# Kernel optimization log

Measured on AMD Instinct MI355X. Metric: run time of the kernel, lower is better.

The kernel has to match this reference:

```python
import jax, jax.numpy as jnp
import numpy as np

NUM_HEADS = 8

def setup_inputs() -> dict:
    key0 = jax.random.key(0)
    ks = jax.random.split(key0, 12)
    L, S, N, E, Dh = 1024, 1024, 8, 512, 64
    w_scale = 1.0 / np.sqrt(E)
    return {
        "query": jax.random.normal(ks[0], (L, N, E), jnp.float32),
        "key": jax.random.normal(ks[1], (S, N, E), jnp.float32),
        "value": jax.random.normal(ks[2], (S, N, E), jnp.float32),
        "pos_k": jax.random.normal(ks[3], (L, S, Dh), jnp.float32) * 0.1,
        "pos_v": jax.random.normal(ks[4], (L, S, Dh), jnp.float32) * 0.1,
        "Wq": jax.random.normal(ks[5], (E, E), jnp.float32) * w_scale,
        "bq": jnp.zeros((E,), jnp.float32),
        "Wk": jax.random.normal(ks[6], (E, E), jnp.float32) * w_scale,
        "bk": jnp.zeros((E,), jnp.float32),
        "Wv": jax.random.normal(ks[7], (E, E), jnp.float32) * w_scale,
        "bv": jnp.zeros((E,), jnp.float32),
        "Wo": jax.random.normal(ks[8], (E, E), jnp.float32) * w_scale,
        "bo": jnp.zeros((E,), jnp.float32),
    }


def reference(query, key, value, pos_k, pos_v, Wq, bq, Wk, bk, Wv, bv, Wo, bo):
    L, N, E = query.shape
    S = key.shape[0]
    H = NUM_HEADS
    Dh = E // H
    scaling = Dh ** -0.5

    # separate Q/K/V projections (torch Linear: x @ W.T + b)
    q = (query @ Wq.T + bq) * scaling          # (L, N, E)
    k = key @ Wk.T + bk                        # (S, N, E)
    v = value @ Wv.T + bv                      # (S, N, E)

    # (L, N*H, Dh) -> (N*H, L, Dh), matching torch's view+transpose
    q = q.reshape(L, N * H, Dh).transpose(1, 0, 2)
    k = k.reshape(S, N * H, Dh).transpose(1, 0, 2)
    v = v.reshape(S, N * H, Dh).transpose(1, 0, 2)

    # content scores + relative-position key term B
    scores = jnp.einsum('bld,bsd->bls', q, k)          # (N*H, L, S)
    scores = scores + jnp.einsum('bld,lsd->bls', q, pos_k)

    # mine_softmax: clamp to finfo.min (turns -inf into finite min), then softmax
    scores = jnp.maximum(scores, jnp.finfo(scores.dtype).min)
    w = jax.nn.softmax(scores, axis=-1)                # (N*H, L, S)

    # attention output + relative-position value term
    out = jnp.einsum('bls,bsd->bld', w, v) + jnp.einsum('bls,lsd->bld', w, pos_v)
    out = out.transpose(1, 0, 2).reshape(L, N, E)
    attn_output = out @ Wo.T + bo                      # (L, N, E)

    # averaged attention weights over heads: (N, L, S)
    avg_w = w.reshape(N, H, L, S).sum(axis=1) / H
    return attn_output, avg_w
```

## Files before the change

### kernel.cpp

```cpp
#include <hip/hip_runtime.h>
#include <hip/hip_bf16.h>
#include <hip/hip_fp16.h>


typedef float     f32x4  __attribute__((ext_vector_type(4)));
typedef _Float16  f16x8  __attribute__((ext_vector_type(8)));

#define MFMA_F16  __builtin_amdgcn_mfma_f32_16x16x32_f16

__device__ __forceinline__ f16x8 ld8f(const float* __restrict__ p){
  const f32x4 a = *(const f32x4*)p;
  const f32x4 b = *(const f32x4*)(p + 4);
  f16x8 h;
#pragma unroll
  for (int t = 0; t < 4; ++t) { h[t] = (_Float16)a[t]; h[t + 4] = (_Float16)b[t]; }
  return h;
}

__device__ __forceinline__ f16x8 cvt8(f32x4 a, f32x4 b){
  f16x8 h;
#pragma unroll
  for (int t = 0; t < 4; ++t) { h[t] = (_Float16)a[t]; h[t + 4] = (_Float16)b[t]; }
  return h;
}

__global__ __launch_bounds__(256) void proj_all(
    const float* __restrict__ Xq, const float* __restrict__ Xk, const float* __restrict__ Xv,
    const float* __restrict__ Wq, const float* __restrict__ Wk, const float* __restrict__ Wv,
    const float* __restrict__ bq, const float* __restrict__ bk, const float* __restrict__ bv,
    _Float16* __restrict__ qb, _Float16* __restrict__ kb, _Float16* __restrict__ vT)
{
  __shared__ _Float16 As[128][40];
  __shared__ _Float16 Bs[128][40];

  const int which = blockIdx.z;
  const float* X    = (which == 0) ? Xq : (which == 1) ? Xk : Xv;
  const float* W    = (which == 0) ? Wq : (which == 1) ? Wk : Wv;
  const float* bias = (which == 0) ? bq : (which == 1) ? bk : bv;
  _Float16*   out   = (which == 0) ? qb : (which == 1) ? kb : vT;
  const float scale = (which == 0) ? 0.125f : 1.0f;
  const int   mode  = (which == 2) ? 1 : 0;

  const int tid = threadIdx.x, wave = tid >> 6, lane = tid & 63;
  const int lrow = lane & 15, quad = lane >> 4;
  const int wr = wave >> 1, wc = wave & 1;
  const int m_base = blockIdx.x * 128;
  const int n_base = blockIdx.y * 128;
  const int srow = tid >> 2, scol = (tid & 3) * 8;

  const float* xp0 = X + (size_t)(m_base + srow)      * 512 + scol;
  const float* xp1 = X + (size_t)(m_base + 64 + srow) * 512 + scol;
  const float* wp0 = W + (size_t)(n_base + srow)      * 512 + scol;
  const float* wp1 = W + (size_t)(n_base + 64 + srow) * 512 + scol;

  f32x4 ra0, ra1, rb0, rb1, rc0, rc1, rd0, rd1;
  auto LOADK = [&](int k0) {
    ra0 = *(const f32x4*)(xp0 + k0);  ra1 = *(const f32x4*)(xp0 + k0 + 4);
    rb0 = *(const f32x4*)(xp1 + k0);  rb1 = *(const f32x4*)(xp1 + k0 + 4);
    rc0 = *(const f32x4*)(wp0 + k0);  rc1 = *(const f32x4*)(wp0 + k0 + 4);
    rd0 = *(const f32x4*)(wp1 + k0);  rd1 = *(const f32x4*)(wp1 + k0 + 4);
  };

  f32x4 acc[4][4] = {};
  LOADK(0);
  for (int k0 = 0; k0 < 512; k0 += 32) {
    __syncthreads();
    *(f16x8*)&As[srow][scol]      = cvt8(ra0, ra1);
    *(f16x8*)&As[srow + 64][scol] = cvt8(rb0, rb1);
    *(f16x8*)&Bs[srow][scol]      = cvt8(rc0, rc1);
    *(f16x8*)&Bs[srow + 64][scol] = cvt8(rd0, rd1);
    __syncthreads();
    if (k0 + 32 < 512) LOADK(k0 + 32);
    f16x8 af[4], bf[4];
#pragma unroll
    for (int mi = 0; mi < 4; ++mi)
      af[mi] = *(const f16x8*)&As[wr * 64 + mi * 16 + lrow][quad * 8];
#pragma unroll
    for (int ni = 0; ni < 4; ++ni)
      bf[ni] = *(const f16x8*)&Bs[wc * 64 + ni * 16 + lrow][quad * 8];
#pragma unroll
    for (int mi = 0; mi < 4; ++mi)
#pragma unroll
      for (int ni = 0; ni < 4; ++ni)
        acc[mi][ni] = MFMA_F16(af[mi], bf[ni], acc[mi][ni], 0, 0, 0);
  }

#pragma unroll
  for (int mi = 0; mi < 4; ++mi)
#pragma unroll
  for (int ni = 0; ni < 4; ++ni) {
    const int ncol = n_base + wc * 64 + ni * 16 + lrow;
    const float bv2 = bias[ncol];
#pragma unroll
    for (int r = 0; r < 4; ++r) {
      const int m = m_base + wr * 64 + mi * 16 + quad * 4 + r;
      const float val = (acc[mi][ni][r] + bv2) * scale;
      if (mode == 0) {
        out[(size_t)m * 512 + ncol] = (_Float16)val;
      } else {
        const int s = m >> 3, nn = m & 7, h = ncol >> 6, d = ncol & 63;
        out[(size_t)(nn * 8 + h) * 65536 + (size_t)d * 1024 + s] = (_Float16)val;
      }
    }
  }
}

__global__ __launch_bounds__(256) void out_gemm(
    const _Float16* __restrict__ X, const float* __restrict__ W,
    const float* __restrict__ bias, float* __restrict__ out)
{
  __shared__ _Float16 As[128][40];
  __shared__ _Float16 Bs[128][40];

  const int tid = threadIdx.x, wave = tid >> 6, lane = tid & 63;
  const int lrow = lane & 15, quad = lane >> 4;
  const int wr = wave >> 1, wc = wave & 1;
  const int m_base = blockIdx.x * 128;
  const int n_base = blockIdx.y * 128;
  const int srow = tid >> 2, scol = (tid & 3) * 8;

  const _Float16* xp0 = X + (size_t)(m_base + srow)      * 512 + scol;
  const _Float16* xp1 = X + (size_t)(m_base + 64 + srow) * 512 + scol;
  const float*    wp0 = W + (size_t)(n_base + srow)      * 512 + scol;
  const float*    wp1 = W + (size_t)(n_base + 64 + srow) * 512 + scol;

  f16x8 ha, hb; f32x4 rc0, rc1, rd0, rd1;
  auto LOADK = [&](int k0) {
    ha  = *(const f16x8*)(xp0 + k0);
    hb  = *(const f16x8*)(xp1 + k0);
    rc0 = *(const f32x4*)(wp0 + k0);  rc1 = *(const f32x4*)(wp0 + k0 + 4);
    rd0 = *(const f32x4*)(wp1 + k0);  rd1 = *(const f32x4*)(wp1 + k0 + 4);
  };

  f32x4 acc[4][4] = {};
  LOADK(0);
  for (int k0 = 0; k0 < 512; k0 += 32) {
    __syncthreads();
    *(f16x8*)&As[srow][scol]      = ha;
    *(f16x8*)&As[srow + 64][scol] = hb;
    *(f16x8*)&Bs[srow][scol]      = cvt8(rc0, rc1);
    *(f16x8*)&Bs[srow + 64][scol] = cvt8(rd0, rd1);
    __syncthreads();
    if (k0 + 32 < 512) LOADK(k0 + 32);
    f16x8 af[4], bf[4];
#pragma unroll
    for (int mi = 0; mi < 4; ++mi)
      af[mi] = *(const f16x8*)&As[wr * 64 + mi * 16 + lrow][quad * 8];
#pragma unroll
    for (int ni = 0; ni < 4; ++ni)
      bf[ni] = *(const f16x8*)&Bs[wc * 64 + ni * 16 + lrow][quad * 8];
#pragma unroll
    for (int mi = 0; mi < 4; ++mi)
#pragma unroll
      for (int ni = 0; ni < 4; ++ni)
        acc[mi][ni] = MFMA_F16(af[mi], bf[ni], acc[mi][ni], 0, 0, 0);
  }

#pragma unroll
  for (int mi = 0; mi < 4; ++mi)
#pragma unroll
  for (int ni = 0; ni < 4; ++ni) {
    const int ncol = n_base + wc * 64 + ni * 16 + lrow;
    const float bv2 = bias[ncol];
#pragma unroll
    for (int r = 0; r < 4; ++r) {
      const int m = m_base + wr * 64 + mi * 16 + quad * 4 + r;
      out[(size_t)m * 512 + ncol] = acc[mi][ni][r] + bv2;
    }
  }
}

__global__ __launch_bounds__(256) void qk_pos(
    const _Float16* __restrict__ qb, const float* __restrict__ pk,
    _Float16* __restrict__ sbuf)
{
  const int l = blockIdx.x;
  const int tid = threadIdx.x, wave = tid >> 6, lane = tid & 63;
  const int lrow = lane & 15, quad = lane >> 4;
  const int b_base = (wave >> 1) * 32;
  const int s_base = blockIdx.y * 64 + (wave & 1) * 32;
  const _Float16* qp = qb + (size_t)l * 4096;
  const float* pp = pk + (size_t)l * 65536;
  f32x4 acc[2][2] = {};
#pragma unroll
  for (int k0 = 0; k0 < 64; k0 += 32) {
    const int ko = k0 + quad * 8;
    f16x8 a0 = *(const f16x8*)(qp + (size_t)(b_base + lrow) * 64 + ko);
    f16x8 a1 = *(const f16x8*)(qp + (size_t)(b_base + 16 + lrow) * 64 + ko);
    f16x8 b0 = ld8f(pp + (size_t)(s_base + lrow) * 64 + ko);
    f16x8 b1 = ld8f(pp + (size_t)(s_base + 16 + lrow) * 64 + ko);
    acc[0][0] = MFMA_F16(a0, b0, acc[0][0], 0, 0, 0);
    acc[0][1] = MFMA_F16(a0, b1, acc[0][1], 0, 0, 0);
    acc[1][0] = MFMA_F16(a1, b0, acc[1][0], 0, 0, 0);
    acc[1][1] = MFMA_F16(a1, b1, acc[1][1], 0, 0, 0);
  }
#pragma unroll
  for (int i = 0; i < 2; ++i)
#pragma unroll
  for (int j = 0; j < 2; ++j)
#pragma unroll
  for (int r = 0; r < 4; ++r) {
    const size_t idx = (size_t)(b_base + i * 16 + quad * 4 + r) * 1048576 +
                       (size_t)l * 1024 + s_base + j * 16 + lrow;
    sbuf[idx] = (_Float16)acc[i][j][r];
  }
}

__global__ __launch_bounds__(256) void qk_content(
    const _Float16* __restrict__ qb, const _Float16* __restrict__ kb,
    _Float16* __restrict__ sbuf)
{
  const int b = blockIdx.z;
  const int tid = threadIdx.x, wave = tid >> 6, lane = tid & 63;
  const int lrow = lane & 15, quad = lane >> 4;
  const int l_base = blockIdx.x * 64 + (wave >> 1) * 32;
  const int s_base = blockIdx.y * 64 + (wave & 1) * 32;
  const _Float16* qp = qb + b * 64;
  const _Float16* kp = kb + b * 64;
  f32x4 acc[2][2] = {};
#pragma unroll
  for (int k0 = 0; k0 < 64; k0 += 32) {
    const int ko = k0 + quad * 8;
    f16x8 a0 = *(const f16x8*)(qp + (size_t)(l_base + lrow) * 4096 + ko);
    f16x8 a1 = *(const f16x8*)(qp + (size_t)(l_base + 16 + lrow) * 4096 + ko);
    f16x8 b0 = *(const f16x8*)(kp + (size_t)(s_base + lrow) * 4096 + ko);
    f16x8 b1 = *(const f16x8*)(kp + (size_t)(s_base + 16 + lrow) * 4096 + ko);
    acc[0][0] = MFMA_F16(a0, b0, acc[0][0], 0, 0, 0);
    acc[0][1] = MFMA_F16(a0, b1, acc[0][1], 0, 0, 0);
    acc[1][0] = MFMA_F16(a1, b0, acc[1][0], 0, 0, 0);
    acc[1][1] = MFMA_F16(a1, b1, acc[1][1], 0, 0, 0);
  }
  _Float16* sp = sbuf + (size_t)b * 1048576;
#pragma unroll
  for (int i = 0; i < 2; ++i)
#pragma unroll
  for (int j = 0; j < 2; ++j)
#pragma unroll
  for (int r = 0; r < 4; ++r) {
    const size_t idx = (size_t)(l_base + i * 16 + quad * 4 + r) * 1024 +
                       s_base + j * 16 + lrow;
    sp[idx] = (_Float16)((float)sp[idx] + acc[i][j][r]);
  }
}

__global__ __launch_bounds__(512) void softmax_avg(
    _Float16* __restrict__ sbuf, float* __restrict__ avg_out)
{
  __shared__ _Float16 lds[8 * 1088];
  const int bx = blockIdx.x;
  const int n = bx >> 10, l = bx & 1023;
  const int tid = threadIdx.x, h = tid >> 6, lane = tid & 63;
  _Float16* row = sbuf + (size_t)(n * 8 + h) * 1048576 + (size_t)l * 1024;
  const f16x8 r0 = *(const f16x8*)(row + lane * 8);
  const f16x8 r1 = *(const f16x8*)(row + 512 + lane * 8);
  float x[16];
#pragma unroll
  for (int t = 0; t < 8; ++t) { x[t] = (float)r0[t]; x[8 + t] = (float)r1[t]; }
  float m = x[0];
#pragma unroll
  for (int i = 1; i < 16; ++i) m = fmaxf(m, x[i]);
#pragma unroll
  for (int off = 32; off > 0; off >>= 1) m = fmaxf(m, __shfl_xor(m, off));
  float z = 0.f;
#pragma unroll
  for (int i = 0; i < 16; ++i) { x[i] = __expf(x[i] - m); z += x[i]; }
#pragma unroll
  for (int off = 32; off > 0; off >>= 1) z += __shfl_xor(z, off);
  const float inv = 1.0f / z;
  f16x8 w0, w1;
#pragma unroll
  for (int t = 0; t < 8; ++t) {
    w0[t] = (_Float16)(x[t] * inv);
    w1[t] = (_Float16)(x[8 + t] * inv);
  }
  *(f16x8*)(row + lane * 8) = w0;
  *(f16x8*)(row + 512 + lane * 8) = w1;
  *(f16x8*)(&lds[h * 1088 + lane * 8]) = w0;
  *(f16x8*)(&lds[h * 1088 + 512 + lane * 8]) = w1;
  __syncthreads();
  float* ao = avg_out + (size_t)n * 1048576 + (size_t)l * 1024;
  for (int s = tid; s < 1024; s += 512) {
    float acc = 0.f;
#pragma unroll
    for (int h2 = 0; h2 < 8; ++h2) acc += (float)lds[h2 * 1088 + s];
    ao[s] = acc * 0.125f;
  }
}

__global__ __launch_bounds__(256) void pv_content(
    const _Float16* __restrict__ sbuf, const _Float16* __restrict__ vT,
    float* __restrict__ ctx)
{
  const int b = blockIdx.x;
  const int tid = threadIdx.x, wave = tid >> 6, lane = tid & 63;
  const int lrow = lane & 15, quad = lane >> 4;
  const int l_base = blockIdx.y * 64 + (wave >> 1) * 32;
  const int d_base = (wave & 1) * 32;
  const _Float16* wp = sbuf + (size_t)b * 1048576;
  const _Float16* vp = vT + (size_t)b * 65536;
  f32x4 acc[2][2] = {};
  for (int s0 = 0; s0 < 1024; s0 += 32) {
    const int so = s0 + quad * 8;
    f16x8 a0 = *(const f16x8*)(wp + (size_t)(l_base + lrow) * 1024 + so);
    f16x8 a1 = *(const f16x8*)(wp + (size_t)(l_base + 16 + lrow) * 1024 + so);
    f16x8 b0 = *(const f16x8*)(vp + (size_t)(d_base + lrow) * 1024 + so);
    f16x8 b1 = *(const f16x8*)(vp + (size_t)(d_base + 16 + lrow) * 1024 + so);
    acc[0][0] = MFMA_F16(a0, b0, acc[0][0], 0, 0, 0);
    acc[0][1] = MFMA_F16(a0, b1, acc[0][1], 0, 0, 0);
    acc[1][0] = MFMA_F16(a1, b0, acc[1][0], 0, 0, 0);
    acc[1][1] = MFMA_F16(a1, b1, acc[1][1], 0, 0, 0);
  }
#pragma unroll
  for (int i = 0; i < 2; ++i)
#pragma unroll
  for (int j = 0; j < 2; ++j)
#pragma unroll
  for (int r = 0; r < 4; ++r)
    ctx[(size_t)(l_base + i * 16 + quad * 4 + r) * 4096 + b * 64 + d_base + j * 16 + lrow] =
        acc[i][j][r];
}

__global__ __launch_bounds__(256) void pv_pos(
    const _Float16* __restrict__ sbuf, const float* __restrict__ pv,
    const float* __restrict__ ctx, _Float16* __restrict__ ctx2)
{
  __shared__ _Float16 lds[64][72];
  const int l = blockIdx.x;
  const int tid = threadIdx.x, wave = tid >> 6, lane = tid & 63;
  const int lrow = lane & 15, quad = lane >> 4;
  const int b_base = (wave >> 1) * 32;
  const int d_base = (wave & 1) * 32;
  const float* pp = pv + (size_t)l * 65536;
  const _Float16* wp = sbuf + (size_t)l * 1024;
  const int st_s = tid >> 2, st_d = (tid & 3) * 16;
  f32x4 acc[2][2] = {};
  for (int s0 = 0; s0 < 1024; s0 += 64) {
    __syncthreads();
    const float* src = pp + (size_t)(s0 + st_s) * 64 + st_d;
    const f32x4 va = *(const f32x4*)src;
    const f32x4 vb = *(const f32x4*)(src + 4);
    const f32x4 vc = *(const f32x4*)(src + 8);
    const f32x4 vd = *(const f32x4*)(src + 12);
#pragma unroll
    for (int u = 0; u < 4; ++u) {
      lds[st_d + u     ][st_s] = (_Float16)va[u];
      lds[st_d + u + 4 ][st_s] = (_Float16)vb[u];
      lds[st_d + u + 8 ][st_s] = (_Float16)vc[u];
      lds[st_d + u + 12][st_s] = (_Float16)vd[u];
    }
    __syncthreads();
#pragma unroll
    for (int k0 = 0; k0 < 64; k0 += 32) {
      const int so = s0 + k0 + quad * 8;
      const int sl = k0 + quad * 8;
      f16x8 a0 = *(const f16x8*)(wp + (size_t)(b_base + lrow) * 1048576 + so);
      f16x8 a1 = *(const f16x8*)(wp + (size_t)(b_base + 16 + lrow) * 1048576 + so);
      f16x8 b0 = *(const f16x8*)(&lds[d_base + lrow][sl]);
      f16x8 b1 = *(const f16x8*)(&lds[d_base + 16 + lrow][sl]);
      acc[0][0] = MFMA_F16(a0, b0, acc[0][0], 0, 0, 0);
      acc[0][1] = MFMA_F16(a0, b1, acc[0][1], 0, 0, 0);
      acc[1][0] = MFMA_F16(a1, b0, acc[1][0], 0, 0, 0);
      acc[1][1] = MFMA_F16(a1, b1, acc[1][1], 0, 0, 0);
    }
  }
#pragma unroll
  for (int i = 0; i < 2; ++i)
#pragma unroll
  for (int j = 0; j < 2; ++j)
#pragma unroll
  for (int r = 0; r < 4; ++r) {
    const size_t idx = (size_t)l * 4096 + (size_t)(b_base + i * 16 + quad * 4 + r) * 64 +
                       d_base + j * 16 + lrow;
    ctx2[idx] = (_Float16)(ctx[idx] + acc[i][j][r]);
  }
}

extern "C" void kernel_launch(void* const* d_in, const int* in_sizes, int n_in,
                              void* d_out, int out_size, void* d_ws, size_t ws_size,
                              hipStream_t stream)
{
  const float* query = (const float*)d_in[0];
  const float* key   = (const float*)d_in[1];
  const float* value = (const float*)d_in[2];
  const float* pos_k = (const float*)d_in[3];
  const float* pos_v = (const float*)d_in[4];
  const float* Wq = (const float*)d_in[5];
  const float* bq = (const float*)d_in[6];
  const float* Wk = (const float*)d_in[7];
  const float* bk = (const float*)d_in[8];
  const float* Wv = (const float*)d_in[9];
  const float* bv = (const float*)d_in[10];
  const float* Wo = (const float*)d_in[11];
  const float* bo = (const float*)d_in[12];

  char* ws = (char*)d_ws;
  _Float16* qb   = (_Float16*)(ws);
  _Float16* kb   = (_Float16*)(ws + (size_t)(8u  << 20));
  _Float16* vT   = (_Float16*)(ws + (size_t)(16u << 20));
  _Float16* sbuf = (_Float16*)(ws + (size_t)(24u << 20));
  float*    ctx  = (float*)   (ws + (size_t)(152u << 20));
  _Float16* ctx2 = (_Float16*)(ws + (size_t)(168u << 20));

  float* out0 = (float*)d_out;
  float* avg  = out0 + (size_t)4194304;

  dim3 blk(256);
  proj_all<<<dim3(64, 4, 3), blk, 0, stream>>>(query, key, value,
                                               Wq, Wk, Wv, bq, bk, bv,
                                               qb, kb, vT);
  qk_pos<<<dim3(1024, 16), blk, 0, stream>>>(qb, pos_k, sbuf);
  qk_content<<<dim3(16, 16, 64), blk, 0, stream>>>(qb, kb, sbuf);
  softmax_avg<<<dim3(8192), dim3(512), 0, stream>>>(sbuf, avg);
  pv_content<<<dim3(64, 16), blk, 0, stream>>>(sbuf, vT, ctx);
  pv_pos<<<dim3(1024), blk, 0, stream>>>(sbuf, pos_v, ctx, ctx2);
  out_gemm<<<dim3(64, 4), blk, 0, stream>>>(ctx2, Wo, bo, out0);
}
```

Baseline: 1.000 ms.

## Loop qk_pos over all S tiles per block with double-buffered pos_k loads

After: 956.8 us. -4.4%, faster.

```diff
diff --git a/kernel.cpp b/kernel.cpp
--- a/kernel.cpp
+++ b/kernel.cpp
@@ -178,31 +178,61 @@
   const int tid = threadIdx.x, wave = tid >> 6, lane = tid & 63;
   const int lrow = lane & 15, quad = lane >> 4;
   const int b_base = (wave >> 1) * 32;
-  const int s_base = blockIdx.y * 64 + (wave & 1) * 32;
+  const int s_half = (wave & 1) * 32;
   const _Float16* qp = qb + (size_t)l * 4096;
   const float* pp = pk + (size_t)l * 65536;
-  f32x4 acc[2][2] = {};
-#pragma unroll
-  for (int k0 = 0; k0 < 64; k0 += 32) {
-    const int ko = k0 + quad * 8;
-    f16x8 a0 = *(const f16x8*)(qp + (size_t)(b_base + lrow) * 64 + ko);
-    f16x8 a1 = *(const f16x8*)(qp + (size_t)(b_base + 16 + lrow) * 64 + ko);
-    f16x8 b0 = ld8f(pp + (size_t)(s_base + lrow) * 64 + ko);
-    f16x8 b1 = ld8f(pp + (size_t)(s_base + 16 + lrow) * 64 + ko);
-    acc[0][0] = MFMA_F16(a0, b0, acc[0][0], 0, 0, 0);
-    acc[0][1] = MFMA_F16(a0, b1, acc[0][1], 0, 0, 0);
-    acc[1][0] = MFMA_F16(a1, b0, acc[1][0], 0, 0, 0);
-    acc[1][1] = MFMA_F16(a1, b1, acc[1][1], 0, 0, 0);
-  }
-#pragma unroll
-  for (int i = 0; i < 2; ++i)
-#pragma unroll
-  for (int j = 0; j < 2; ++j)
-#pragma unroll
-  for (int r = 0; r < 4; ++r) {
-    const size_t idx = (size_t)(b_base + i * 16 + quad * 4 + r) * 1048576 +
-                       (size_t)l * 1024 + s_base + j * 16 + lrow;
-    sbuf[idx] = (_Float16)acc[i][j][r];
+
+  f16x8 a[2][2];
+#pragma unroll
+  for (int ks = 0; ks < 2; ++ks) {
+    const int ko = ks * 32 + quad * 8;
+    a[ks][0] = *(const f16x8*)(qp + (size_t)(b_base + lrow) * 64 + ko);
+    a[ks][1] = *(const f16x8*)(qp + (size_t)(b_base + 16 + lrow) * 64 + ko);
+  }
+
+  auto LOADS = [&](int s0, f32x4 (&buf)[8]) {
+#pragma unroll
+    for (int ks = 0; ks < 2; ++ks) {
+      const int ko = ks * 32 + quad * 8;
+      const float* r0 = pp + (size_t)(s0 + s_half + lrow) * 64 + ko;
+      const float* r1 = r0 + 16 * 64;
+      buf[ks * 4 + 0] = *(const f32x4*)r0;
+      buf[ks * 4 + 1] = *(const f32x4*)(r0 + 4);
+      buf[ks * 4 + 2] = *(const f32x4*)r1;
+      buf[ks * 4 + 3] = *(const f32x4*)(r1 + 4);
+    }
+  };
+
+  auto COMPUTE = [&](int s0, f32x4 (&buf)[8]) {
+    f32x4 acc[2][2] = {};
+#pragma unroll
+    for (int ks = 0; ks < 2; ++ks) {
+      const f16x8 b0 = cvt8(buf[ks * 4 + 0], buf[ks * 4 + 1]);
+      const f16x8 b1 = cvt8(buf[ks * 4 + 2], buf[ks * 4 + 3]);
+      acc[0][0] = MFMA_F16(a[ks][0], b0, acc[0][0], 0, 0, 0);
+      acc[0][1] = MFMA_F16(a[ks][0], b1, acc[0][1], 0, 0, 0);
+      acc[1][0] = MFMA_F16(a[ks][1], b0, acc[1][0], 0, 0, 0);
+      acc[1][1] = MFMA_F16(a[ks][1], b1, acc[1][1], 0, 0, 0);
+    }
+#pragma unroll
+    for (int i = 0; i < 2; ++i)
+#pragma unroll
+    for (int j = 0; j < 2; ++j)
+#pragma unroll
+    for (int r = 0; r < 4; ++r) {
+      const size_t idx = (size_t)(b_base + i * 16 + quad * 4 + r) * 1048576 +
+                         (size_t)l * 1024 + s0 + s_half + j * 16 + lrow;
+      sbuf[idx] = (_Float16)acc[i][j][r];
+    }
+  };
+
+  f32x4 bufA[8], bufB[8];
+  LOADS(0, bufA);
+  for (int s0 = 0; s0 < 1024; s0 += 128) {
+    LOADS(s0 + 64, bufB);
+    COMPUTE(s0, bufA);
+    if (s0 + 128 < 1024) LOADS(s0 + 128, bufA);
+    COMPUTE(s0 + 64, bufB);
   }
 }
 
@@ -408,7 +438,7 @@
   proj_all<<<dim3(64, 4, 3), blk, 0, stream>>>(query, key, value,
                                                Wq, Wk, Wv, bq, bk, bv,
                                                qb, kb, vT);
-  qk_pos<<<dim3(1024, 16), blk, 0, stream>>>(qb, pos_k, sbuf);
+  qk_pos<<<dim3(1024), blk, 0, stream>>>(qb, pos_k, sbuf);
   qk_content<<<dim3(16, 16, 64), blk, 0, stream>>>(qb, kb, sbuf);
   softmax_avg<<<dim3(8192), dim3(512), 0, stream>>>(sbuf, avg);
   pv_content<<<dim3(64, 16), blk, 0, stream>>>(sbuf, vT, ctx);
```

## Fuse positional-key scores into softmax/average kernel and relayout score buffer l-major

Applied to the files above, without the earlier changes.

Result: faster. 954.3 us (-4.6%).

```diff
diff --git a/kernel.cpp b/kernel.cpp
--- a/kernel.cpp
+++ b/kernel.cpp
@@ -5,6 +5,7 @@
 
 typedef float     f32x4  __attribute__((ext_vector_type(4)));
 typedef _Float16  f16x8  __attribute__((ext_vector_type(8)));
+typedef _Float16  f16x4  __attribute__((ext_vector_type(4)));
 
 #define MFMA_F16  __builtin_amdgcn_mfma_f32_16x16x32_f16
 
@@ -167,42 +168,6 @@
       const int m = m_base + wr * 64 + mi * 16 + quad * 4 + r;
       out[(size_t)m * 512 + ncol] = acc[mi][ni][r] + bv2;
     }
-  }
-}
-
-__global__ __launch_bounds__(256) void qk_pos(
-    const _Float16* __restrict__ qb, const float* __restrict__ pk,
-    _Float16* __restrict__ sbuf)
-{
-  const int l = blockIdx.x;
-  const int tid = threadIdx.x, wave = tid >> 6, lane = tid & 63;
-  const int lrow = lane & 15, quad = lane >> 4;
-  const int b_base = (wave >> 1) * 32;
-  const int s_base = blockIdx.y * 64 + (wave & 1) * 32;
-  const _Float16* qp = qb + (size_t)l * 4096;
-  const float* pp = pk + (size_t)l * 65536;
-  f32x4 acc[2][2] = {};
-#pragma unroll
-  for (int k0 = 0; k0 < 64; k0 += 32) {
-    const int ko = k0 + quad * 8;
-    f16x8 a0 = *(const f16x8*)(qp + (size_t)(b_base + lrow) * 64 + ko);
-    f16x8 a1 = *(const f16x8*)(qp + (size_t)(b_base + 16 + lrow) * 64 + ko);
-    f16x8 b0 = ld8f(pp + (size_t)(s_base + lrow) * 64 + ko);
-    f16x8 b1 = ld8f(pp + (size_t)(s_base + 16 + lrow) * 64 + ko);
-    acc[0][0] = MFMA_F16(a0, b0, acc[0][0], 0, 0, 0);
-    acc[0][1] = MFMA_F16(a0, b1, acc[0][1], 0, 0, 0);
-    acc[1][0] = MFMA_F16(a1, b0, acc[1][0], 0, 0, 0);
-    acc[1][1] = MFMA_F16(a1, b1, acc[1][1], 0, 0, 0);
-  }
-#pragma unroll
-  for (int i = 0; i < 2; ++i)
-#pragma unroll
-  for (int j = 0; j < 2; ++j)
-#pragma unroll
-  for (int r = 0; r < 4; ++r) {
-    const size_t idx = (size_t)(b_base + i * 16 + quad * 4 + r) * 1048576 +
-                       (size_t)l * 1024 + s_base + j * 16 + lrow;
-    sbuf[idx] = (_Float16)acc[i][j][r];
   }
 }
 
@@ -230,60 +195,106 @@
     acc[1][0] = MFMA_F16(a1, b0, acc[1][0], 0, 0, 0);
     acc[1][1] = MFMA_F16(a1, b1, acc[1][1], 0, 0, 0);
   }
-  _Float16* sp = sbuf + (size_t)b * 1048576;
 #pragma unroll
   for (int i = 0; i < 2; ++i)
 #pragma unroll
   for (int j = 0; j < 2; ++j)
 #pragma unroll
   for (int r = 0; r < 4; ++r) {
-    const size_t idx = (size_t)(l_base + i * 16 + quad * 4 + r) * 1024 +
-                       s_base + j * 16 + lrow;
-    sp[idx] = (_Float16)((float)sp[idx] + acc[i][j][r]);
-  }
-}
-
-__global__ __launch_bounds__(512) void softmax_avg(
+    const size_t idx = (size_t)(l_base + i * 16 + quad * 4 + r) * 65536 +
+                       (size_t)b * 1024 + s_base + j * 16 + lrow;
+    sbuf[idx] = (_Float16)acc[i][j][r];
+  }
+}
+
+__global__ __launch_bounds__(512, 4) void pos_softmax_avg(
+    const _Float16* __restrict__ qb, const float* __restrict__ pk,
     _Float16* __restrict__ sbuf, float* __restrict__ avg_out)
 {
-  __shared__ _Float16 lds[8 * 1088];
-  const int bx = blockIdx.x;
-  const int n = bx >> 10, l = bx & 1023;
-  const int tid = threadIdx.x, h = tid >> 6, lane = tid & 63;
-  _Float16* row = sbuf + (size_t)(n * 8 + h) * 1048576 + (size_t)l * 1024;
-  const f16x8 r0 = *(const f16x8*)(row + lane * 8);
-  const f16x8 r1 = *(const f16x8*)(row + 512 + lane * 8);
-  float x[16];
-#pragma unroll
-  for (int t = 0; t < 8; ++t) { x[t] = (float)r0[t]; x[8 + t] = (float)r1[t]; }
-  float m = x[0];
-#pragma unroll
-  for (int i = 1; i < 16; ++i) m = fmaxf(m, x[i]);
-#pragma unroll
-  for (int off = 32; off > 0; off >>= 1) m = fmaxf(m, __shfl_xor(m, off));
-  float z = 0.f;
-#pragma unroll
-  for (int i = 0; i < 16; ++i) { x[i] = __expf(x[i] - m); z += x[i]; }
-#pragma unroll
-  for (int off = 32; off > 0; off >>= 1) z += __shfl_xor(z, off);
-  const float inv = 1.0f / z;
-  f16x8 w0, w1;
-#pragma unroll
-  for (int t = 0; t < 8; ++t) {
-    w0[t] = (_Float16)(x[t] * inv);
-    w1[t] = (_Float16)(x[8 + t] * inv);
-  }
-  *(f16x8*)(row + lane * 8) = w0;
-  *(f16x8*)(row + 512 + lane * 8) = w1;
-  *(f16x8*)(&lds[h * 1088 + lane * 8]) = w0;
-  *(f16x8*)(&lds[h * 1088 + 512 + lane * 8]) = w1;
+  __shared__ float pmax[2][4][16];
+  __shared__ float psum[2][4][16];
+
+  const int l = blockIdx.x;
+  const int bh = blockIdx.y;
+  const int tid = threadIdx.x, wave = tid >> 6, lane = tid & 63;
+  const int lrow = lane & 15, quad = lane >> 4;
+  const int wb = wave >> 2;
+  const int ws = wave & 3;
+  const int b0 = bh * 32 + wb * 16;
+
+  const _Float16* qp = qb + (size_t)l * 4096 + (size_t)b0 * 64;
+  const float*    pp = pk + (size_t)l * 65536 + (size_t)(ws * 256) * 64;
+  _Float16*       sp = sbuf + (size_t)l * 65536;
+
+  f16x8 bq[2];
+#pragma unroll
+  for (int ks = 0; ks < 2; ++ks)
+    bq[ks] = *(const f16x8*)(qp + (size_t)lrow * 64 + ks * 32 + quad * 8);
+
+  f32x4 acc[16] = {};
+#pragma unroll
+  for (int t = 0; t < 16; ++t) {
+#pragma unroll
+    for (int ks = 0; ks < 2; ++ks) {
+      const f16x8 a = ld8f(pp + (size_t)(t * 16 + lrow) * 64 + ks * 32 + quad * 8);
+      acc[t] = MFMA_F16(a, bq[ks], acc[t], 0, 0, 0);
+    }
+  }
+
+  const _Float16* crow = sp + (size_t)(b0 + lrow) * 1024 + ws * 256 + quad * 4;
+#pragma unroll
+  for (int t = 0; t < 16; ++t) {
+    const f16x4 c = *(const f16x4*)(crow + t * 16);
+#pragma unroll
+    for (int r = 0; r < 4; ++r) acc[t][r] += (float)c[r];
+  }
+
+  float mw = acc[0][0];
+#pragma unroll
+  for (int t = 0; t < 16; ++t)
+#pragma unroll
+    for (int r = 0; r < 4; ++r) mw = fmaxf(mw, acc[t][r]);
+  mw = fmaxf(mw, __shfl_xor(mw, 16));
+  mw = fmaxf(mw, __shfl_xor(mw, 32));
+
+  float zw = 0.f;
+#pragma unroll
+  for (int t = 0; t < 16; ++t)
+#pragma unroll
+    for (int r = 0; r < 4; ++r) { acc[t][r] = __expf(acc[t][r] - mw); zw += acc[t][r]; }
+  zw += __shfl_xor(zw, 16);
+  zw += __shfl_xor(zw, 32);
+
+  if (lane < 16) { pmax[wb][ws][lrow] = mw; psum[wb][ws][lrow] = zw; }
   __syncthreads();
-  float* ao = avg_out + (size_t)n * 1048576 + (size_t)l * 1024;
-  for (int s = tid; s < 1024; s += 512) {
-    float acc = 0.f;
-#pragma unroll
-    for (int h2 = 0; h2 < 8; ++h2) acc += (float)lds[h2 * 1088 + s];
-    ao[s] = acc * 0.125f;
+
+  float M = pmax[wb][0][lrow];
+#pragma unroll
+  for (int o = 1; o < 4; ++o) M = fmaxf(M, pmax[wb][o][lrow]);
+  float Z = 0.f;
+#pragma unroll
+  for (int o = 0; o < 4; ++o) Z += psum[wb][o][lrow] * __expf(pmax[wb][o][lrow] - M);
+  const float scl = __expf(mw - M) / Z;
+
+  _Float16* wrow = sp + (size_t)(b0 + lrow) * 1024 + ws * 256 + quad * 4;
+  const int n = (b0 + lrow) >> 3;
+  float* ao = avg_out + (size_t)n * 1048576 + (size_t)l * 1024 + ws * 256 + quad * 4;
+  const bool wr_avg = ((lane & 7) == 0);
+#pragma unroll
+  for (int t = 0; t < 16; ++t) {
+    f16x4 wv; f32x4 av;
+#pragma unroll
+    for (int r = 0; r < 4; ++r) {
+      const float w = acc[t][r] * scl;
+      wv[r] = (_Float16)w;
+      float hsum = w;
+      hsum += __shfl_xor(hsum, 1);
+      hsum += __shfl_xor(hsum, 2);
+      hsum += __shfl_xor(hsum, 4);
+      av[r] = hsum * 0.125f;
+    }
+    *(f16x4*)(wrow + t * 16) = wv;
+    if (wr_avg) *(f32x4*)(ao + t * 16) = av;
   }
 }
 
@@ -296,13 +307,13 @@
   const int lrow = lane & 15, quad = lane >> 4;
   const int l_base = blockIdx.y * 64 + (wave >> 1) * 32;
   const int d_base = (wave & 1) * 32;
-  const _Float16* wp = sbuf + (size_t)b * 1048576;
+  const _Float16* wp = sbuf + (size_t)b * 1024;
   const _Float16* vp = vT + (size_t)b * 65536;
   f32x4 acc[2][2] = {};
   for (int s0 = 0; s0 < 1024; s0 += 32) {
     const int so = s0 + quad * 8;
-    f16x8 a0 = *(const f16x8*)(wp + (size_t)(l_base + lrow) * 1024 + so);
-    f16x8 a1 = *(const f16x8*)(wp + (size_t)(l_base + 16 + lrow) * 1024 + so);
+    f16x8 a0 = *(const f16x8*)(wp + (size_t)(l_base + lrow) * 65536 + so);
+    f16x8 a1 = *(const f16x8*)(wp + (size_t)(l_base + 16 + lrow) * 65536 + so);
     f16x8 b0 = *(const f16x8*)(vp + (size_t)(d_base + lrow) * 1024 + so);
     f16x8 b1 = *(const f16x8*)(vp + (size_t)(d_base + 16 + lrow) * 1024 + so);
     acc[0][0] = MFMA_F16(a0, b0, acc[0][0], 0, 0, 0);
@@ -331,7 +342,7 @@
   const int b_base = (wave >> 1) * 32;
   const int d_base = (wave & 1) * 32;
   const float* pp = pv + (size_t)l * 65536;
-  const _Float16* wp = sbuf + (size_t)l * 1024;
+  const _Float16* wp = sbuf + (size_t)l * 65536;
   const int st_s = tid >> 2, st_d = (tid & 3) * 16;
   f32x4 acc[2][2] = {};
   for (int s0 = 0; s0 < 1024; s0 += 64) {
@@ -353,8 +364,8 @@
     for (int k0 = 0; k0 < 64; k0 += 32) {
       const int so = s0 + k0 + quad * 8;
       const int sl = k0 + quad * 8;
-      f16x8 a0 = *(const f16x8*)(wp + (size_t)(b_base + lrow) * 1048576 + so);
-      f16x8 a1 = *(const f16x8*)(wp + (size_t)(b_base + 16 + lrow) * 1048576 + so);
+      f16x8 a0 = *(const f16x8*)(wp + (size_t)(b_base + lrow) * 1024 + so);
+      f16x8 a1 = *(const f16x8*)(wp + (size_t)(b_base + 16 + lrow) * 1024 + so);
       f16x8 b0 = *(const f16x8*)(&lds[d_base + lrow][sl]);
       f16x8 b1 = *(const f16x8*)(&lds[d_base + 16 + lrow][sl]);
       acc[0][0] = MFMA_F16(a0, b0, acc[0][0], 0, 0, 0);
@@ -408,9 +419,8 @@
   proj_all<<<dim3(64, 4, 3), blk, 0, stream>>>(query, key, value,
                                                Wq, Wk, Wv, bq, bk, bv,
                                                qb, kb, vT);
-  qk_pos<<<dim3(1024, 16), blk, 0, stream>>>(qb, pos_k, sbuf);
   qk_content<<<dim3(16, 16, 64), blk, 0, stream>>>(qb, kb, sbuf);
-  softmax_avg<<<dim3(8192), dim3(512), 0, stream>>>(sbuf, avg);
+  pos_softmax_avg<<<dim3(1024, 2), dim3(512), 0, stream>>>(qb, pos_k, sbuf, avg);
   pv_content<<<dim3(64, 16), blk, 0, stream>>>(sbuf, vT, ctx);
   pv_pos<<<dim3(1024), blk, 0, stream>>>(sbuf, pos_v, ctx, ctx2);
   out_gemm<<<dim3(64, 4), blk, 0, stream>>>(ctx2, Wo, bo, out0);
```
